# Kernel tuning notes

Measured on AMD Instinct MI355X. Metric: run time of the kernel, lower is better.

Reference implementation:

```python
import jax, jax.numpy as jnp
import numpy as np

WIN = 32  # window_size


def _groupnorm(x, w, b, eps=1e-5):
    # GroupNorm(1, dim): normalize over (C, W, H) per sample, per-channel affine
    mu = x.mean(axis=(1, 2, 3), keepdims=True)
    var = x.var(axis=(1, 2, 3), keepdims=True)
    xh = (x - mu) * jax.lax.rsqrt(var + eps)
    return xh * w[None, :, None, None] + b[None, :, None, None]


def setup_inputs() -> dict:
    key = jax.random.key(0)
    ks = jax.random.split(key, 7)
    B, C, W, H = 2, 1, 64, 1024
    d = 32
    x = jax.random.normal(ks[0], (B, C, W, H), jnp.float32)
    # 1x1 convs == per-pixel linear maps; store weights as [out, in]
    w_in = jax.random.normal(ks[1], (d, C), jnp.float32) * 0.5
    w_q = jax.random.normal(ks[2], (d, d), jnp.float32) * d ** -0.5
    w_k = jax.random.normal(ks[3], (d, d), jnp.float32) * d ** -0.5
    w_v = jax.random.normal(ks[4], (d, d), jnp.float32) * d ** -0.5
    w_out = jax.random.normal(ks[5], (C, d), jnp.float32) * d ** -0.5
    gn_w = jnp.ones((d,), jnp.float32)
    gn_b = jnp.zeros((d,), jnp.float32)
    gamma = jnp.array(1.0, jnp.float32)
    return {"x": x, "w_in": w_in, "w_q": w_q, "w_k": w_k, "w_v": w_v,
            "w_out": w_out, "gn_w": gn_w, "gn_b": gn_b, "gamma": gamma}


def reference(x, w_in, w_q, w_k, w_v, w_out, gn_w, gn_b, gamma):
    B, C, W, H = x.shape
    d = w_in.shape[0]
    scale = d ** -0.5

    feat = jnp.einsum('bcwh,dc->bdwh', x, w_in)              # in_proj (1x1 conv)
    z = jax.nn.gelu(_groupnorm(feat, gn_w, gn_b), approximate=False)
    q = jnp.einsum('bdwh,ed->bewh', z, w_q)
    k = jnp.einsum('bdwh,ed->bewh', z, w_k)
    v = jnp.einsum('bdwh,ed->bewh', z, w_v)

    def rows(t):  # [B,d,W,H] -> [B*W, H, d]
        return t.transpose(0, 2, 3, 1).reshape(B * W, H, d)

    q, k, v = rows(q), rows(k), rows(v)

    attn = jnp.einsum('nid,njd->nij', q * scale, k)          # [N, H, H]
    idx = jnp.arange(H)
    band = jnp.abs(idx[None, :] - idx[:, None]) <= WIN       # True = visible
    attn = jnp.where(band[None], attn, jnp.finfo(attn.dtype).min)
    attn = jax.nn.softmax(attn, axis=-1)

    o = jnp.einsum('nij,njd->nid', attn, v)                  # [N, H, d]
    o = o.reshape(B, W, H, d).transpose(0, 3, 1, 2)          # [B, d, W, H]

    out = feat + gamma * o
    out = jax.nn.gelu(_groupnorm(out, gn_w, gn_b), approximate=False)
    return jnp.einsum('bdwh,cd->bcwh', out, w_out)           # out_proj
```

## Files before the change

kernel.cpp:

```cpp
#include <hip/hip_runtime.h>
#include <hip/hip_fp16.h>
#include <cmath>

#define H_DIM 1024
#define DCH 32
#define WINR 32
#define TQ 256
#define HALO (TQ + 2*WINR)
#define NBLK 512

__device__ __forceinline__ float gelu_f(float v) {
    return 0.5f * v * (1.0f + erff(v * 0.70710678118654752440f));
}

__device__ __forceinline__ int sxof(int p) { return (p & 3) ^ ((p >> 2) & 3); }

union H2U { unsigned u; __half2 h; };

__device__ __forceinline__ unsigned pack2(float a, float b) {
    H2U cv; cv.h = __floats2half2_rn(a, b); return cv.u;
}

__device__ __forceinline__ float dot8(uint4 kc, const float* qp) {
    H2U a, b, c, d; a.u = kc.x; b.u = kc.y; c.u = kc.z; d.u = kc.w;
    float2 k0 = __half22float2(a.h), k1 = __half22float2(b.h);
    float2 k2 = __half22float2(c.h), k3 = __half22float2(d.h);
    float r = 0.f;
    r = fmaf(k0.x, qp[0], r); r = fmaf(k0.y, qp[1], r);
    r = fmaf(k1.x, qp[2], r); r = fmaf(k1.y, qp[3], r);
    r = fmaf(k2.x, qp[4], r); r = fmaf(k2.y, qp[5], r);
    r = fmaf(k3.x, qp[6], r); r = fmaf(k3.y, qp[7], r);
    return r;
}

__device__ __forceinline__ void pv8(uint4 vc, float pw, float* o8) {
    H2U a, b, c, d; a.u = vc.x; b.u = vc.y; c.u = vc.z; d.u = vc.w;
    float2 v0 = __half22float2(a.h), v1 = __half22float2(b.h);
    float2 v2 = __half22float2(c.h), v3 = __half22float2(d.h);
    o8[0] = fmaf(pw, v0.x, o8[0]); o8[1] = fmaf(pw, v0.y, o8[1]);
    o8[2] = fmaf(pw, v1.x, o8[2]); o8[3] = fmaf(pw, v1.y, o8[3]);
    o8[4] = fmaf(pw, v2.x, o8[4]); o8[5] = fmaf(pw, v2.y, o8[5]);
    o8[6] = fmaf(pw, v3.x, o8[6]); o8[7] = fmaf(pw, v3.y, o8[7]);
}

__device__ __forceinline__ void write_row_h(uint4* buf, int p, const float r[DCH]) {
    const int sx = sxof(p);
    #pragma unroll
    for (int c = 0; c < 4; ++c) {
        uint4 w;
        w.x = pack2(r[8*c+0], r[8*c+1]);
        w.y = pack2(r[8*c+2], r[8*c+3]);
        w.z = pack2(r[8*c+4], r[8*c+5]);
        w.w = pack2(r[8*c+6], r[8*c+7]);
        buf[p * 4 + (c ^ sx)] = w;
    }
}

__device__ __forceinline__ void matvec32(const float* __restrict__ w,
                                         const float zv[DCH], float out[DCH]) {
    #pragma unroll
    for (int e = 0; e < DCH; ++e) {
        const float* wr = w + e * DCH;
        float a0 = 0.f, a1 = 0.f, a2 = 0.f, a3 = 0.f;
        #pragma unroll
        for (int d = 0; d < DCH; d += 4) {
            a0 = fmaf(zv[d+0], wr[d+0], a0);
            a1 = fmaf(zv[d+1], wr[d+1], a1);
            a2 = fmaf(zv[d+2], wr[d+2], a2);
            a3 = fmaf(zv[d+3], wr[d+3], a3);
        }
        out[e] = (a0 + a1) + (a2 + a3);
    }
}

__global__ __launch_bounds__(256) void k_xstats(const float* __restrict__ x,
                                                double* __restrict__ part) {
    __shared__ double red[8];
    const int b = blockIdx.x;
    const int t = threadIdx.x;
    const float4* px = (const float4*)(x + (size_t)b * 8192);
    double s = 0.0, s2 = 0.0;
    #pragma unroll
    for (int i = 0; i < 8; ++i) {
        float4 v = px[i * 256 + t];
        s  += (double)v.x + (double)v.y + (double)v.z + (double)v.w;
        s2 += (double)v.x*v.x + (double)v.y*v.y + (double)v.z*v.z + (double)v.w*v.w;
    }
    #pragma unroll
    for (int o = 32; o; o >>= 1) { s += __shfl_down(s, o); s2 += __shfl_down(s2, o); }
    if ((t & 63) == 0) { red[(t>>6)*2] = s; red[(t>>6)*2+1] = s2; }
    __syncthreads();
    if (t == 0) {
        part[b*2+0] = red[0]+red[2]+red[4]+red[6];
        part[b*2+1] = red[1]+red[3]+red[5]+red[7];
    }
}

__global__ __launch_bounds__(256, 2) void k_main(
    const float* __restrict__ x,
    const float* __restrict__ w_in,
    const float* __restrict__ w_q,
    const float* __restrict__ w_k,
    const float* __restrict__ w_v,
    const float* __restrict__ gn_w,
    const float* __restrict__ gn_b,
    const float* __restrict__ gammap,
    const double* __restrict__ xpart,
    double* __restrict__ gn2part,
    float* __restrict__ out_pre)
{
    __shared__ uint4 ks4[HALO * 4];
    __shared__ uint4 vs4[HALO * 4];

    const int t     = threadIdx.x;
    const int bid   = blockIdx.x;
    const int row   = bid >> 2;
    const int tile  = bid & 3;
    const int batch = row >> 6;
    const int h0    = tile * TQ;
    const int g0    = h0 - WINR;

    double Sx = 0.0, Sx2 = 0.0;
    const double* bp = xpart + batch * 16;
    #pragma unroll
    for (int i = 0; i < 8; ++i) { Sx += bp[2*i]; Sx2 += bp[2*i+1]; }
    float sw = 0.f, sw2 = 0.f;
    #pragma unroll
    for (int d = 0; d < DCH; ++d) { float w = w_in[d]; sw += w; sw2 += w*w; }
    const double n1   = 2097152.0;
    const double mu1d = (double)sw * Sx / n1;
    const double var1 = (double)sw2 * Sx2 / n1 - mu1d * mu1d;
    const float  mu1  = (float)mu1d;
    const float  rstd1 = (float)(1.0 / sqrt(var1 + 1e-5));

    float ca[DCH], cb[DCH];
    #pragma unroll
    for (int d = 0; d < DCH; ++d) {
        float a = rstd1 * gn_w[d];
        ca[d] = w_in[d] * a;
        cb[d] = gn_b[d] - mu1 * a;
    }

    const float* xrow = x + (size_t)row * H_DIM;

    const float xq = xrow[h0 + t];
    float q[DCH];
    {
        float zv[DCH];
        #pragma unroll
        for (int d = 0; d < DCH; ++d) zv[d] = gelu_f(fmaf(xq, ca[d], cb[d]));
        float kr[DCH], vr[DCH];
        matvec32(w_k, zv, kr);
        matvec32(w_v, zv, vr);
        write_row_h(ks4, t + WINR, kr);
        write_row_h(vs4, t + WINR, vr);
        matvec32(w_q, zv, q);
        #pragma unroll
        for (int e = 0; e < DCH; ++e) q[e] *= 0.17677669529663688f;
    }
    if (t < 64) {
        const int p0 = (t < 32) ? t : (256 + t);
        const int h  = g0 + p0;
        const float xv = ((unsigned)h < H_DIM) ? xrow[h] : 0.f;
        float zv[DCH];
        #pragma unroll
        for (int d = 0; d < DCH; ++d) zv[d] = gelu_f(fmaf(xv, ca[d], cb[d]));
        float kr[DCH], vr[DCH];
        matvec32(w_k, zv, kr);
        matvec32(w_v, zv, vr);
        write_row_h(ks4, p0, kr);
        write_row_h(vs4, p0, vr);
    }
    __syncthreads();

    const int lane  = t & 63;
    const int wid   = t >> 6;
    const int pbase = wid * 64;
    const int jbase = g0 + pbase;

    float m = -80.0f, l = 0.f;
    float o[DCH];
    #pragma unroll
    for (int d = 0; d < DCH; ++d) o[d] = 0.f;

    #pragma unroll 2
    for (int ch = 0; ch < 16; ++ch) {
        float sc[8];
        #pragma unroll
        for (int u = 0; u < 8; ++u) {
            const int kk = ch * 8 + u;
            const int p  = pbase + kk;
            const int sx = sxof(p);
            const uint4* kb = ks4 + p * 4;
            uint4 c0 = kb[0 ^ sx];
            uint4 c1 = kb[1 ^ sx];
            uint4 c2 = kb[2 ^ sx];
            uint4 c3 = kb[3 ^ sx];
            const float s = (dot8(c0, q) + dot8(c1, q + 8)) +
                            (dot8(c2, q + 16) + dot8(c3, q + 24));
            const bool valid = ((unsigned)(kk - lane) <= 64u) &&
                               ((unsigned)(jbase + kk) < (unsigned)H_DIM);
            sc[u] = valid ? s : -3.0e38f;
        }
        const float c01 = fmaxf(sc[0], sc[1]);
        const float c23 = fmaxf(sc[2], sc[3]);
        const float c45 = fmaxf(sc[4], sc[5]);
        const float c67 = fmaxf(sc[6], sc[7]);
        const float cmax = fmaxf(fmaxf(c01, c23), fmaxf(c45, c67));
        if (__any(cmax > m + 8.0f)) {
            const float mn = fmaxf(m, cmax);
            const float corr = __expf(m - mn);
            l *= corr;
            #pragma unroll
            for (int d = 0; d < DCH; ++d) o[d] *= corr;
            m = mn;
        }
        #pragma unroll
        for (int u = 0; u < 8; ++u) {
            const float pw = __expf(sc[u] - m);
            l += pw;
            const int p  = pbase + ch * 8 + u;
            const int sx = sxof(p);
            const uint4* vb = vs4 + p * 4;
            pv8(vb[0 ^ sx], pw, o + 0);
            pv8(vb[1 ^ sx], pw, o + 8);
            pv8(vb[2 ^ sx], pw, o + 16);
            pv8(vb[3 ^ sx], pw, o + 24);
        }
    }
    const float inv = 1.0f / l;

    const float gamma = gammap[0];
    float so = 0.f, so2 = 0.f;
    float* op = out_pre + ((size_t)row * H_DIM + (h0 + t)) * DCH;
    #pragma unroll
    for (int c = 0; c < 8; ++c) {
        float4 wi4 = ((const float4*)w_in)[c];
        float4 r;
        r.x = fmaf(gamma, o[4*c+0] * inv, xq * wi4.x);
        r.y = fmaf(gamma, o[4*c+1] * inv, xq * wi4.y);
        r.z = fmaf(gamma, o[4*c+2] * inv, xq * wi4.z);
        r.w = fmaf(gamma, o[4*c+3] * inv, xq * wi4.w);
        ((float4*)op)[c] = r;
        so  += r.x + r.y + r.z + r.w;
        so2 += r.x*r.x + r.y*r.y + r.z*r.z + r.w*r.w;
    }
    double ds = (double)so, ds2 = (double)so2;
    #pragma unroll
    for (int ofs = 32; ofs; ofs >>= 1) {
        ds  += __shfl_down(ds, ofs);
        ds2 += __shfl_down(ds2, ofs);
    }
    __syncthreads();
    double* red = (double*)ks4;
    if (lane == 0) { red[wid*2] = ds; red[wid*2+1] = ds2; }
    __syncthreads();
    if (t == 0) {
        gn2part[bid*2+0] = red[0]+red[2]+red[4]+red[6];
        gn2part[bid*2+1] = red[1]+red[3]+red[5]+red[7];
    }
}

__global__ __launch_bounds__(256) void k_out(
    const float* __restrict__ out_pre,
    const float* __restrict__ w_out,
    const float* __restrict__ gn_w,
    const float* __restrict__ gn_b,
    const double* __restrict__ gn2part,
    float* __restrict__ outp)
{
    __shared__ double red[8];
    const int t   = threadIdx.x;
    const int bid = blockIdx.x;
    const int batch = bid >> 8;

    const double* gp = gn2part + (size_t)batch * 512;
    double ds = gp[2*t], ds2 = gp[2*t+1];
    #pragma unroll
    for (int ofs = 32; ofs; ofs >>= 1) {
        ds  += __shfl_down(ds, ofs);
        ds2 += __shfl_down(ds2, ofs);
    }
    if ((t & 63) == 0) { red[(t>>6)*2] = ds; red[(t>>6)*2+1] = ds2; }
    __syncthreads();
    const double S  = red[0]+red[2]+red[4]+red[6];
    const double S2 = red[1]+red[3]+red[5]+red[7];
    const double n2 = 2097152.0;
    const double mu = S / n2;
    const double var = S2 / n2 - mu * mu;
    const float muf  = (float)mu;
    const float rstd = (float)(1.0 / sqrt(var + 1e-5));

    const int pix = bid * 256 + t;
    const float4* ip = (const float4*)(out_pre + (size_t)pix * DCH);
    float acc_o = 0.f;
    #pragma unroll
    for (int c = 0; c < 8; ++c) {
        float4 v  = ip[c];
        float4 gw = ((const float4*)gn_w)[c];
        float4 gb = ((const float4*)gn_b)[c];
        float4 wo = ((const float4*)w_out)[c];
        acc_o += gelu_f((v.x - muf) * rstd * gw.x + gb.x) * wo.x;
        acc_o += gelu_f((v.y - muf) * rstd * gw.y + gb.y) * wo.y;
        acc_o += gelu_f((v.z - muf) * rstd * gw.z + gb.z) * wo.z;
        acc_o += gelu_f((v.w - muf) * rstd * gw.w + gb.w) * wo.w;
    }
    outp[pix] = acc_o;
}

extern "C" void kernel_launch(void* const* d_in, const int* in_sizes, int n_in,
                              void* d_out, int out_size, void* d_ws, size_t ws_size,
                              hipStream_t stream) {
    const float* x     = (const float*)d_in[0];
    const float* w_in  = (const float*)d_in[1];
    const float* w_q   = (const float*)d_in[2];
    const float* w_k   = (const float*)d_in[3];
    const float* w_v   = (const float*)d_in[4];
    const float* w_out = (const float*)d_in[5];
    const float* gn_w  = (const float*)d_in[6];
    const float* gn_b  = (const float*)d_in[7];
    const float* gamma = (const float*)d_in[8];

    double* xpart   = (double*)d_ws;
    double* gn2part = (double*)((char*)d_ws + 256);
    float*  out_pre = (float*)((char*)d_ws + 8448);
    float*  outp    = (float*)d_out;

    k_xstats<<<dim3(16),   dim3(256), 0, stream>>>(x, xpart);
    k_main  <<<dim3(NBLK), dim3(256), 0, stream>>>(
        x, w_in, w_q, w_k, w_v, gn_w, gn_b, gamma, xpart, gn2part, out_pre);
    k_out   <<<dim3(512),  dim3(256), 0, stream>>>(out_pre, w_out, gn_w, gn_b, gn2part, outp);
}
```

Measured before the change: 208.5 us.

## Split attention key range across two waves per query and merge softmax states

Doubles the main kernel's block size to 512 threads. Each query row's 128-key band is now split between two waves that each process 64 keys, and their online-softmax states are merged through shared memory. K/V projection is assigned one thread per halo position instead of combining the main and edge passes. The goal is to shorten the serial per-thread loop and raise parallelism. The cost is an extra merge step with two barriers, 35-float spills per lane into shared memory, and tighter register limits from launch_bounds(512,4).

```diff
diff --git a/kernel.cpp b/kernel.cpp
--- a/kernel.cpp
+++ b/kernel.cpp
@@ -96,7 +96,7 @@
     }
 }
 
-__global__ __launch_bounds__(256, 2) void k_main(
+__global__ __launch_bounds__(512, 4) void k_main(
     const float* __restrict__ x,
     const float* __restrict__ w_in,
     const float* __restrict__ w_q,
@@ -109,10 +109,14 @@
     double* __restrict__ gn2part,
     float* __restrict__ out_pre)
 {
-    __shared__ uint4 ks4[HALO * 4];
-    __shared__ uint4 vs4[HALO * 4];
+    __shared__ uint4 kv[2][HALO * 4];
+    __shared__ double red[8];
 
     const int t     = threadIdx.x;
+    const int lane  = t & 63;
+    const int wid   = t >> 6;
+    const int qq    = wid & 3;
+    const int kh    = wid >> 2;
     const int bid   = blockIdx.x;
     const int row   = bid >> 2;
     const int tile  = bid & 3;
@@ -143,24 +147,19 @@
 
     const float* xrow = x + (size_t)row * H_DIM;
 
-    const float xq = xrow[h0 + t];
+    const int qidx = qq * 64 + lane;
+    const float xq = xrow[h0 + qidx];
     float q[DCH];
     {
         float zv[DCH];
         #pragma unroll
         for (int d = 0; d < DCH; ++d) zv[d] = gelu_f(fmaf(xq, ca[d], cb[d]));
-        float kr[DCH], vr[DCH];
-        matvec32(w_k, zv, kr);
-        matvec32(w_v, zv, vr);
-        write_row_h(ks4, t + WINR, kr);
-        write_row_h(vs4, t + WINR, vr);
         matvec32(w_q, zv, q);
         #pragma unroll
         for (int e = 0; e < DCH; ++e) q[e] *= 0.17677669529663688f;
     }
-    if (t < 64) {
-        const int p0 = (t < 32) ? t : (256 + t);
-        const int h  = g0 + p0;
+    if (t < HALO) {
+        const int h  = g0 + t;
         const float xv = ((unsigned)h < H_DIM) ? xrow[h] : 0.f;
         float zv[DCH];
         #pragma unroll
@@ -168,15 +167,12 @@
         float kr[DCH], vr[DCH];
         matvec32(w_k, zv, kr);
         matvec32(w_v, zv, vr);
-        write_row_h(ks4, p0, kr);
-        write_row_h(vs4, p0, vr);
-    }
-    __syncthreads();
-
-    const int lane  = t & 63;
-    const int wid   = t >> 6;
-    const int pbase = wid * 64;
-    const int jbase = g0 + pbase;
+        write_row_h(kv[0], t, kr);
+        write_row_h(kv[1], t, vr);
+    }
+    __syncthreads();
+
+    const int pbase = qq * 64 + kh * 64;
 
     float m = -80.0f, l = 0.f;
     float o[DCH];
@@ -184,22 +180,23 @@
     for (int d = 0; d < DCH; ++d) o[d] = 0.f;
 
     #pragma unroll 2
-    for (int ch = 0; ch < 16; ++ch) {
+    for (int ch = 0; ch < 8; ++ch) {
         float sc[8];
         #pragma unroll
         for (int u = 0; u < 8; ++u) {
-            const int kk = ch * 8 + u;
-            const int p  = pbase + kk;
-            const int sx = sxof(p);
-            const uint4* kb = ks4 + p * 4;
+            const int cu8 = ch * 8 + u;
+            const int p   = pbase + cu8;
+            const int sx  = sxof(p);
+            const uint4* kb = kv[0] + p * 4;
             uint4 c0 = kb[0 ^ sx];
             uint4 c1 = kb[1 ^ sx];
             uint4 c2 = kb[2 ^ sx];
             uint4 c3 = kb[3 ^ sx];
             const float s = (dot8(c0, q) + dot8(c1, q + 8)) +
                             (dot8(c2, q + 16) + dot8(c3, q + 24));
-            const bool valid = ((unsigned)(kk - lane) <= 64u) &&
-                               ((unsigned)(jbase + kk) < (unsigned)H_DIM);
+            const int rel = kh * 64 + cu8;
+            const bool valid = ((unsigned)(rel - lane) <= 64u) &&
+                               ((unsigned)(g0 + p) < (unsigned)H_DIM);
             sc[u] = valid ? s : -3.0e38f;
         }
         const float c01 = fmaxf(sc[0], sc[1]);
@@ -221,39 +218,57 @@
             l += pw;
             const int p  = pbase + ch * 8 + u;
             const int sx = sxof(p);
-            const uint4* vb = vs4 + p * 4;
+            const uint4* vb = kv[1] + p * 4;
             pv8(vb[0 ^ sx], pw, o + 0);
             pv8(vb[1 ^ sx], pw, o + 8);
             pv8(vb[2 ^ sx], pw, o + 16);
             pv8(vb[3 ^ sx], pw, o + 24);
         }
     }
-    const float inv = 1.0f / l;
-
-    const float gamma = gammap[0];
-    float so = 0.f, so2 = 0.f;
-    float* op = out_pre + ((size_t)row * H_DIM + (h0 + t)) * DCH;
-    #pragma unroll
-    for (int c = 0; c < 8; ++c) {
-        float4 wi4 = ((const float4*)w_in)[c];
-        float4 r;
-        r.x = fmaf(gamma, o[4*c+0] * inv, xq * wi4.x);
-        r.y = fmaf(gamma, o[4*c+1] * inv, xq * wi4.y);
-        r.z = fmaf(gamma, o[4*c+2] * inv, xq * wi4.z);
-        r.w = fmaf(gamma, o[4*c+3] * inv, xq * wi4.w);
-        ((float4*)op)[c] = r;
-        so  += r.x + r.y + r.z + r.w;
-        so2 += r.x*r.x + r.y*r.y + r.z*r.z + r.w*r.w;
-    }
-    double ds = (double)so, ds2 = (double)so2;
-    #pragma unroll
-    for (int ofs = 32; ofs; ofs >>= 1) {
-        ds  += __shfl_down(ds, ofs);
-        ds2 += __shfl_down(ds2, ofs);
-    }
-    __syncthreads();
-    double* red = (double*)ks4;
-    if (lane == 0) { red[wid*2] = ds; red[wid*2+1] = ds2; }
+
+    __syncthreads();
+    float* mb = (float*)kv;
+    if (kh == 1) {
+        float* dst = mb + (qq * 64 + lane) * 35;
+        dst[0] = m; dst[1] = l;
+        #pragma unroll
+        for (int d = 0; d < DCH; ++d) dst[2 + d] = o[d];
+    }
+    __syncthreads();
+    if (kh == 0) {
+        const float* src = mb + (qq * 64 + lane) * 35;
+        const float m2 = src[0], l2 = src[1];
+        const float mm = fmaxf(m, m2);
+        const float c1 = __expf(m - mm);
+        const float c2 = __expf(m2 - mm);
+        l = l * c1 + l2 * c2;
+        #pragma unroll
+        for (int d = 0; d < DCH; ++d) o[d] = o[d] * c1 + src[2 + d] * c2;
+
+        const float inv = 1.0f / l;
+        const float gamma = gammap[0];
+        float so = 0.f, so2 = 0.f;
+        float* op = out_pre + ((size_t)row * H_DIM + (h0 + qidx)) * DCH;
+        #pragma unroll
+        for (int c = 0; c < 8; ++c) {
+            float4 wi4 = ((const float4*)w_in)[c];
+            float4 r;
+            r.x = fmaf(gamma, o[4*c+0] * inv, xq * wi4.x);
+            r.y = fmaf(gamma, o[4*c+1] * inv, xq * wi4.y);
+            r.z = fmaf(gamma, o[4*c+2] * inv, xq * wi4.z);
+            r.w = fmaf(gamma, o[4*c+3] * inv, xq * wi4.w);
+            ((float4*)op)[c] = r;
+            so  += r.x + r.y + r.z + r.w;
+            so2 += r.x*r.x + r.y*r.y + r.z*r.z + r.w*r.w;
+        }
+        double ds = (double)so, ds2 = (double)so2;
+        #pragma unroll
+        for (int ofs = 32; ofs; ofs >>= 1) {
+            ds  += __shfl_down(ds, ofs);
+            ds2 += __shfl_down(ds2, ofs);
+        }
+        if (lane == 0) { red[qq*2] = ds; red[qq*2+1] = ds2; }
+    }
     __syncthreads();
     if (t == 0) {
         gn2part[bid*2+0] = red[0]+red[2]+red[4]+red[6];
@@ -327,7 +342,7 @@
     float*  outp    = (float*)d_out;
 
     k_xstats<<<dim3(16),   dim3(256), 0, stream>>>(x, xpart);
-    k_main  <<<dim3(NBLK), dim3(256), 0, stream>>>(
+    k_main  <<<dim3(NBLK), dim3(512), 0, stream>>>(
         x, w_in, w_q, w_k, w_v, gn_w, gn_b, gamma, xpart, gn2part, out_pre);
     k_out   <<<dim3(512),  dim3(256), 0, stream>>>(out_pre, w_out, gn_w, gn_b, gn2part, outp);
 }
```

Measured after the change: 274.7 us. 1.32x slower.

## Split head dim across half-waves and shrink query tiles to raise occupancy

Applied to the files above, without the earlier changes.

Each query is now handled by two lanes, each owning 16 of the 32 channels, and the partial QK dot products are combined with a cross-lane shuffle. Query tiles shrink from 256 to 128, so there are twice as many blocks, and launch bounds allow 4 blocks per CU. The K/V halo rows are built by 192 threads instead of a 256+64 split. Together these halve per-thread register arrays and aim for more occupancy and parallelism, at the cost of redundant z/GELU computation per lane pair, an extra shuffle per score, and more halo recomputation relative to tile size.

```diff
diff --git a/kernel.cpp b/kernel.cpp
--- a/kernel.cpp
+++ b/kernel.cpp
@@ -5,15 +5,13 @@
 #define H_DIM 1024
 #define DCH 32
 #define WINR 32
-#define TQ 256
-#define HALO (TQ + 2*WINR)
-#define NBLK 512
+#define QB 128
+#define HALO2 192
+#define NQ 131072
 
 __device__ __forceinline__ float gelu_f(float v) {
     return 0.5f * v * (1.0f + erff(v * 0.70710678118654752440f));
 }
-
-__device__ __forceinline__ int sxof(int p) { return (p & 3) ^ ((p >> 2) & 3); }
 
 union H2U { unsigned u; __half2 h; };
 
@@ -43,24 +41,11 @@
     o8[6] = fmaf(pw, v3.x, o8[6]); o8[7] = fmaf(pw, v3.y, o8[7]);
 }
 
-__device__ __forceinline__ void write_row_h(uint4* buf, int p, const float r[DCH]) {
-    const int sx = sxof(p);
-    #pragma unroll
-    for (int c = 0; c < 4; ++c) {
-        uint4 w;
-        w.x = pack2(r[8*c+0], r[8*c+1]);
-        w.y = pack2(r[8*c+2], r[8*c+3]);
-        w.z = pack2(r[8*c+4], r[8*c+5]);
-        w.w = pack2(r[8*c+6], r[8*c+7]);
-        buf[p * 4 + (c ^ sx)] = w;
-    }
-}
-
-__device__ __forceinline__ void matvec32(const float* __restrict__ w,
-                                         const float zv[DCH], float out[DCH]) {
-    #pragma unroll
-    for (int e = 0; e < DCH; ++e) {
-        const float* wr = w + e * DCH;
+__device__ __forceinline__ void matvec16(const float* __restrict__ w, int ebase,
+                                         const float zv[DCH], float out[16]) {
+    #pragma unroll
+    for (int e = 0; e < 16; ++e) {
+        const float* wr = w + (ebase + e) * DCH;
         float a0 = 0.f, a1 = 0.f, a2 = 0.f, a3 = 0.f;
         #pragma unroll
         for (int d = 0; d < DCH; d += 4) {
@@ -73,6 +58,20 @@
     }
 }
 
+__device__ __forceinline__ int cpos(int p, int c) { return p * 4 + (c ^ (p & 3)); }
+
+__device__ __forceinline__ void make_z(float xv, float mu1, float rstd1,
+                                       const float* __restrict__ w_in,
+                                       const float* __restrict__ gn_w,
+                                       const float* __restrict__ gn_b,
+                                       float zv[DCH]) {
+    #pragma unroll
+    for (int d = 0; d < DCH; ++d) {
+        float a = rstd1 * gn_w[d];
+        zv[d] = gelu_f(fmaf(xv, w_in[d] * a, gn_b[d] - mu1 * a));
+    }
+}
+
 __global__ __launch_bounds__(256) void k_xstats(const float* __restrict__ x,
                                                 double* __restrict__ part) {
     __shared__ double red[8];
@@ -96,7 +95,7 @@
     }
 }
 
-__global__ __launch_bounds__(256, 2) void k_main(
+__global__ __launch_bounds__(256, 4) void k_main(
     const float* __restrict__ x,
     const float* __restrict__ w_in,
     const float* __restrict__ w_q,
@@ -109,16 +108,18 @@
     double* __restrict__ gn2part,
     float* __restrict__ out_pre)
 {
-    __shared__ uint4 ks4[HALO * 4];
-    __shared__ uint4 vs4[HALO * 4];
-
-    const int t     = threadIdx.x;
-    const int bid   = blockIdx.x;
-    const int row   = bid >> 2;
-    const int tile  = bid & 3;
+    __shared__ uint4 kv[2][HALO2 * 4];
+    __shared__ double red[8];
+
+    const int t    = threadIdx.x;
+    const int lane = t & 63;
+    const int w    = t >> 6;
+    const int ql   = lane & 31;
+    const int dh   = lane >> 5;
+    const int bid  = blockIdx.x;
+    const int row  = bid >> 3;
+    const int qb   = (bid & 7) * QB;
     const int batch = row >> 6;
-    const int h0    = tile * TQ;
-    const int g0    = h0 - WINR;
 
     double Sx = 0.0, Sx2 = 0.0;
     const double* bp = xpart + batch * 16;
@@ -126,116 +127,106 @@
     for (int i = 0; i < 8; ++i) { Sx += bp[2*i]; Sx2 += bp[2*i+1]; }
     float sw = 0.f, sw2 = 0.f;
     #pragma unroll
-    for (int d = 0; d < DCH; ++d) { float w = w_in[d]; sw += w; sw2 += w*w; }
+    for (int d = 0; d < DCH; ++d) { float wv = w_in[d]; sw += wv; sw2 += wv*wv; }
     const double n1   = 2097152.0;
     const double mu1d = (double)sw * Sx / n1;
     const double var1 = (double)sw2 * Sx2 / n1 - mu1d * mu1d;
     const float  mu1  = (float)mu1d;
     const float  rstd1 = (float)(1.0 / sqrt(var1 + 1e-5));
 
-    float ca[DCH], cb[DCH];
-    #pragma unroll
-    for (int d = 0; d < DCH; ++d) {
-        float a = rstd1 * gn_w[d];
-        ca[d] = w_in[d] * a;
-        cb[d] = gn_b[d] - mu1 * a;
-    }
-
     const float* xrow = x + (size_t)row * H_DIM;
 
-    const float xq = xrow[h0 + t];
-    float q[DCH];
+    if (t < HALO2) {
+        const int h = qb - WINR + t;
+        const float xv = ((unsigned)h < H_DIM) ? xrow[h] : 0.f;
+        float zv[DCH];
+        make_z(xv, mu1, rstd1, w_in, gn_w, gn_b, zv);
+        float r16[16];
+        matvec16(w_k, 0,  zv, r16);
+        kv[0][cpos(t,0)] = make_uint4(pack2(r16[0],r16[1]),  pack2(r16[2],r16[3]),
+                                      pack2(r16[4],r16[5]),  pack2(r16[6],r16[7]));
+        kv[0][cpos(t,1)] = make_uint4(pack2(r16[8],r16[9]),  pack2(r16[10],r16[11]),
+                                      pack2(r16[12],r16[13]),pack2(r16[14],r16[15]));
+        matvec16(w_k, 16, zv, r16);
+        kv[0][cpos(t,2)] = make_uint4(pack2(r16[0],r16[1]),  pack2(r16[2],r16[3]),
+                                      pack2(r16[4],r16[5]),  pack2(r16[6],r16[7]));
+        kv[0][cpos(t,3)] = make_uint4(pack2(r16[8],r16[9]),  pack2(r16[10],r16[11]),
+                                      pack2(r16[12],r16[13]),pack2(r16[14],r16[15]));
+        matvec16(w_v, 0,  zv, r16);
+        kv[1][cpos(t,0)] = make_uint4(pack2(r16[0],r16[1]),  pack2(r16[2],r16[3]),
+                                      pack2(r16[4],r16[5]),  pack2(r16[6],r16[7]));
+        kv[1][cpos(t,1)] = make_uint4(pack2(r16[8],r16[9]),  pack2(r16[10],r16[11]),
+                                      pack2(r16[12],r16[13]),pack2(r16[14],r16[15]));
+        matvec16(w_v, 16, zv, r16);
+        kv[1][cpos(t,2)] = make_uint4(pack2(r16[0],r16[1]),  pack2(r16[2],r16[3]),
+                                      pack2(r16[4],r16[5]),  pack2(r16[6],r16[7]));
+        kv[1][cpos(t,3)] = make_uint4(pack2(r16[8],r16[9]),  pack2(r16[10],r16[11]),
+                                      pack2(r16[12],r16[13]),pack2(r16[14],r16[15]));
+    }
+
+    const int qi = w * 32 + ql;
+    const float xq = xrow[qb + qi];
+    float q[16];
     {
         float zv[DCH];
+        make_z(xq, mu1, rstd1, w_in, gn_w, gn_b, zv);
+        matvec16(w_q, dh * 16, zv, q);
         #pragma unroll
-        for (int d = 0; d < DCH; ++d) zv[d] = gelu_f(fmaf(xq, ca[d], cb[d]));
-        float kr[DCH], vr[DCH];
-        matvec32(w_k, zv, kr);
-        matvec32(w_v, zv, vr);
-        write_row_h(ks4, t + WINR, kr);
-        write_row_h(vs4, t + WINR, vr);
-        matvec32(w_q, zv, q);
+        for (int e = 0; e < 16; ++e) q[e] *= 0.17677669529663688f;
+    }
+    __syncthreads();
+
+    const int p0 = w * 32;
+    const int hb = qb - WINR + p0;
+
+    float m = -80.0f, l = 0.f;
+    float o[16];
+    #pragma unroll
+    for (int d = 0; d < 16; ++d) o[d] = 0.f;
+
+    for (int ch = 0; ch < 24; ++ch) {
+        float sc[4];
         #pragma unroll
-        for (int e = 0; e < DCH; ++e) q[e] *= 0.17677669529663688f;
-    }
-    if (t < 64) {
-        const int p0 = (t < 32) ? t : (256 + t);
-        const int h  = g0 + p0;
-        const float xv = ((unsigned)h < H_DIM) ? xrow[h] : 0.f;
-        float zv[DCH];
-        #pragma unroll
-        for (int d = 0; d < DCH; ++d) zv[d] = gelu_f(fmaf(xv, ca[d], cb[d]));
-        float kr[DCH], vr[DCH];
-        matvec32(w_k, zv, kr);
-        matvec32(w_v, zv, vr);
-        write_row_h(ks4, p0, kr);
-        write_row_h(vs4, p0, vr);
-    }
-    __syncthreads();
-
-    const int lane  = t & 63;
-    const int wid   = t >> 6;
-    const int pbase = wid * 64;
-    const int jbase = g0 + pbase;
-
-    float m = -80.0f, l = 0.f;
-    float o[DCH];
-    #pragma unroll
-    for (int d = 0; d < DCH; ++d) o[d] = 0.f;
-
-    #pragma unroll 2
-    for (int ch = 0; ch < 16; ++ch) {
-        float sc[8];
-        #pragma unroll
-        for (int u = 0; u < 8; ++u) {
-            const int kk = ch * 8 + u;
-            const int p  = pbase + kk;
-            const int sx = sxof(p);
-            const uint4* kb = ks4 + p * 4;
-            uint4 c0 = kb[0 ^ sx];
-            uint4 c1 = kb[1 ^ sx];
-            uint4 c2 = kb[2 ^ sx];
-            uint4 c3 = kb[3 ^ sx];
-            const float s = (dot8(c0, q) + dot8(c1, q + 8)) +
-                            (dot8(c2, q + 16) + dot8(c3, q + 24));
-            const bool valid = ((unsigned)(kk - lane) <= 64u) &&
-                               ((unsigned)(jbase + kk) < (unsigned)H_DIM);
+        for (int u = 0; u < 4; ++u) {
+            const int j = ch * 4 + u;
+            const int p = p0 + j;
+            const uint4* kb = kv[0];
+            uint4 c0 = kb[p * 4 + ((2*dh)     ^ (p & 3))];
+            uint4 c1 = kb[p * 4 + ((2*dh + 1) ^ (p & 3))];
+            float partial = dot8(c0, q) + dot8(c1, q + 8);
+            const float s = partial + __shfl_xor(partial, 32);
+            const bool valid = ((unsigned)(j - ql) <= 64u) &&
+                               ((unsigned)(hb + j) < (unsigned)H_DIM);
             sc[u] = valid ? s : -3.0e38f;
         }
-        const float c01 = fmaxf(sc[0], sc[1]);
-        const float c23 = fmaxf(sc[2], sc[3]);
-        const float c45 = fmaxf(sc[4], sc[5]);
-        const float c67 = fmaxf(sc[6], sc[7]);
-        const float cmax = fmaxf(fmaxf(c01, c23), fmaxf(c45, c67));
+        const float cmax = fmaxf(fmaxf(sc[0], sc[1]), fmaxf(sc[2], sc[3]));
         if (__any(cmax > m + 8.0f)) {
             const float mn = fmaxf(m, cmax);
             const float corr = __expf(m - mn);
             l *= corr;
             #pragma unroll
-            for (int d = 0; d < DCH; ++d) o[d] *= corr;
+            for (int d = 0; d < 16; ++d) o[d] *= corr;
             m = mn;
         }
         #pragma unroll
-        for (int u = 0; u < 8; ++u) {
+        for (int u = 0; u < 4; ++u) {
             const float pw = __expf(sc[u] - m);
             l += pw;
-            const int p  = pbase + ch * 8 + u;
-            const int sx = sxof(p);
-            const uint4* vb = vs4 + p * 4;
-            pv8(vb[0 ^ sx], pw, o + 0);
-            pv8(vb[1 ^ sx], pw, o + 8);
-            pv8(vb[2 ^ sx], pw, o + 16);
-            pv8(vb[3 ^ sx], pw, o + 24);
+            const int p = p0 + ch * 4 + u;
+            const uint4* vb = kv[1];
+            pv8(vb[p * 4 + ((2*dh)     ^ (p & 3))], pw, o + 0);
+            pv8(vb[p * 4 + ((2*dh + 1) ^ (p & 3))], pw, o + 8);
         }
     }
     const float inv = 1.0f / l;
 
     const float gamma = gammap[0];
+    const size_t qg = (size_t)bid * QB + qi;
+    float* op = out_pre + qg * DCH + dh * 16;
     float so = 0.f, so2 = 0.f;
-    float* op = out_pre + ((size_t)row * H_DIM + (h0 + t)) * DCH;
-    #pragma unroll
-    for (int c = 0; c < 8; ++c) {
-        float4 wi4 = ((const float4*)w_in)[c];
+    #pragma unroll
+    for (int c = 0; c < 4; ++c) {
+        float4 wi4 = ((const float4*)w_in)[dh * 4 + c];
         float4 r;
         r.x = fmaf(gamma, o[4*c+0] * inv, xq * wi4.x);
         r.y = fmaf(gamma, o[4*c+1] * inv, xq * wi4.y);
@@ -251,9 +242,7 @@
         ds  += __shfl_down(ds, ofs);
         ds2 += __shfl_down(ds2, ofs);
     }
-    __syncthreads();
-    double* red = (double*)ks4;
-    if (lane == 0) { red[wid*2] = ds; red[wid*2+1] = ds2; }
+    if (lane == 0) { red[w*2] = ds; red[w*2+1] = ds2; }
     __syncthreads();
     if (t == 0) {
         gn2part[bid*2+0] = red[0]+red[2]+red[4]+red[6];
@@ -274,8 +263,9 @@
     const int bid = blockIdx.x;
     const int batch = bid >> 8;
 
-    const double* gp = gn2part + (size_t)batch * 512;
-    double ds = gp[2*t], ds2 = gp[2*t+1];
+    const double* gp = gn2part + (size_t)batch * 1024;
+    double ds  = gp[2*t]   + gp[2*t + 512];
+    double ds2 = gp[2*t+1] + gp[2*t + 513];
     #pragma unroll
     for (int ofs = 32; ofs; ofs >>= 1) {
         ds  += __shfl_down(ds, ofs);
@@ -321,13 +311,14 @@
     const float* gn_b  = (const float*)d_in[7];
     const float* gamma = (const float*)d_in[8];
 
-    double* xpart   = (double*)d_ws;
-    double* gn2part = (double*)((char*)d_ws + 256);
-    float*  out_pre = (float*)((char*)d_ws + 8448);
+    char* ws = (char*)d_ws;
+    double* xpart   = (double*)ws;
+    double* gn2part = (double*)(ws + 256);
+    float*  out_pre = (float*)(ws + 256 + 16384);
     float*  outp    = (float*)d_out;
 
     k_xstats<<<dim3(16),   dim3(256), 0, stream>>>(x, xpart);
-    k_main  <<<dim3(NBLK), dim3(256), 0, stream>>>(
+    k_main  <<<dim3(1024), dim3(256), 0, stream>>>(
         x, w_in, w_q, w_k, w_v, gn_w, gn_b, gamma, xpart, gn2part, out_pre);
     k_out   <<<dim3(512),  dim3(256), 0, stream>>>(out_pre, w_out, gn_w, gn_b, gn2part, outp);
 }
```

Measured after the change: 285.6 us. 1.37x slower.
